# Kernel tuning notes

Measured on AMD Instinct MI355X. Metric: run time of the kernel, lower is better.

Reference implementation:

```python
import jax, jax.numpy as jnp
import numpy as np

B, S, D, E, H = 4, 2048, 1024, 8, 4096  # batch, seq, d_model, n_experts, ffn hidden (4*d_model)


def setup_inputs() -> dict:
    key = jax.random.key(0)
    ks = jax.random.split(key, 4)
    s = 0.02  # init scale
    return {
        "x": jax.random.normal(ks[0], (B, S, D), dtype=jnp.float32),
        "router_w": jax.random.normal(ks[1], (E, D), dtype=jnp.float32) * s,
        "router_b": jnp.zeros((E,), dtype=jnp.float32),
        "w1": jax.random.normal(ks[2], (E, D, H), dtype=jnp.float32) * s,
        "b1": jnp.zeros((E, H), dtype=jnp.float32),
        "w2": jax.random.normal(ks[3], (E, H, D), dtype=jnp.float32) * s,
        "b2": jnp.zeros((E, D), dtype=jnp.float32),
        "top_k": 2,
    }


def reference(x, router_w, router_b, w1, b1, w2, b2, top_k):
    # Router logits [B, S, E]
    logits = jnp.einsum('bsd,ed->bse', x, router_w) + router_b
    # Top-k selection; scatter top-k logits into a -inf tensor, then softmax
    # => gate weight is exactly 0 for non-selected experts.
    top_v, top_i = jax.lax.top_k(logits, top_k)           # [B, S, k]
    sel = jax.nn.one_hot(top_i, logits.shape[-1], dtype=bool).any(axis=-2)  # [B, S, E]
    gate = jax.nn.softmax(jnp.where(sel, logits, -jnp.inf), axis=-1)        # [B, S, E]

    # Dense sum over experts (mathematically identical to the masked
    # gather/scatter loop since non-selected gates are exactly 0).
    out = jnp.zeros_like(x)
    for e in range(w1.shape[0]):  # small fixed expert loop keeps peak memory low
        h = jax.nn.relu(x @ w1[e] + b1[e])        # [B, S, H]
        out = out + (h @ w2[e] + b2[e]) * gate[..., e:e + 1]
    return out
```

## Files before the change

kernel.cpp:

```cpp
#include <hip/hip_runtime.h>
#include <hip/hip_bf16.h>

#define NTOK   8192
#define DMODEL 1024
#define NEXP   8
#define HFFN   4096
#define NSLOT  16384
#define MAXWL  72

typedef __bf16 bf16x8 __attribute__((ext_vector_type(8)));
typedef float  f32x4  __attribute__((ext_vector_type(4)));
typedef unsigned short u16;
typedef u16 u16x8 __attribute__((ext_vector_type(8)));

typedef const __attribute__((address_space(1))) void* gas_ptr;
typedef __attribute__((address_space(3))) void* las_ptr;

__device__ inline u16 f2b(float f) {
  __hip_bfloat16 h = __float2bfloat16(f);
  return *reinterpret_cast<u16*>(&h);
}
__device__ inline float b2f(u16 u) {
  unsigned int v = ((unsigned int)u) << 16;
  return *reinterpret_cast<float*>(&v);
}

__global__ void router_k(const float* __restrict__ x, const float* __restrict__ rw,
                         const float* __restrict__ rb, int* __restrict__ tok_e,
                         float* __restrict__ tok_g) {
  int wave = threadIdx.x >> 6, lane = threadIdx.x & 63;
  int t = blockIdx.x * 4 + wave;
  const float* xr = x + (size_t)t * DMODEL;
  float acc[NEXP];
#pragma unroll
  for (int e = 0; e < NEXP; e++) acc[e] = 0.f;
#pragma unroll
  for (int i = 0; i < 4; i++) {
    int d = i * 256 + lane * 4;
    float4 xv = *(const float4*)(xr + d);
#pragma unroll
    for (int e = 0; e < NEXP; e++) {
      float4 wv = *(const float4*)(rw + (size_t)e * DMODEL + d);
      acc[e] += xv.x * wv.x + xv.y * wv.y + xv.z * wv.z + xv.w * wv.w;
    }
  }
#pragma unroll
  for (int e = 0; e < NEXP; e++) {
#pragma unroll
    for (int off = 32; off > 0; off >>= 1) acc[e] += __shfl_xor(acc[e], off);
  }
  if (lane == 0) {
    float lg[NEXP];
#pragma unroll
    for (int e = 0; e < NEXP; e++) lg[e] = acc[e] + rb[e];
    int e0 = 0;
#pragma unroll
    for (int e = 1; e < NEXP; e++) if (lg[e] > lg[e0]) e0 = e;
    int e1 = (e0 == 0) ? 1 : 0;
#pragma unroll
    for (int e = 0; e < NEXP; e++) if (e != e0 && lg[e] > lg[e1]) e1 = e;
    float ex = expf(lg[e1] - lg[e0]);
    float g0 = 1.f / (1.f + ex);
    float g1 = ex / (1.f + ex);
    tok_e[2 * t]     = e0;  tok_e[2 * t + 1] = e1;
    tok_g[2 * t]     = g0;  tok_g[2 * t + 1] = g1;
  }
}

__global__ void count_k(const int* __restrict__ tok_e, int* __restrict__ counts) {
  __shared__ int h[NEXP];
  int tid = threadIdx.x;
  if (tid < NEXP) h[tid] = 0;
  __syncthreads();
  int t = blockIdx.x * 256 + tid;
  atomicAdd(&h[tok_e[2 * t]], 1);
  atomicAdd(&h[tok_e[2 * t + 1]], 1);
  __syncthreads();
  if (tid < NEXP) atomicAdd(&counts[tid], h[tid]);
}

__global__ void offsets_k(const int* __restrict__ counts, int* __restrict__ offsets,
                          int* __restrict__ wl) {
  if (threadIdx.x == 0) {
    int s = 0;
    for (int e = 0; e < NEXP; e++) { offsets[e] = s; s += counts[e]; }
    offsets[NEXP] = s;
    int n = 0;
    for (int e = 0; e < NEXP; e++)
      for (int t = 0; t * 256 < counts[e]; ++t) wl[n++] = (e << 16) | t;
    for (int i = n; i < MAXWL; ++i) wl[i] = -1;
  }
}

__global__ void assign_k(const int* __restrict__ tok_e, int* __restrict__ cursors,
                         const int* __restrict__ offsets, int* __restrict__ row_tok,
                         int* __restrict__ slot_of) {
  __shared__ int h[NEXP], base[NEXP];
  int tid = threadIdx.x;
  if (tid < NEXP) h[tid] = 0;
  __syncthreads();
  int t = blockIdx.x * 256 + tid;
  int e0 = tok_e[2 * t], e1 = tok_e[2 * t + 1];
  int r0 = atomicAdd(&h[e0], 1);
  int r1 = atomicAdd(&h[e1], 1);
  __syncthreads();
  if (tid < NEXP) base[tid] = atomicAdd(&cursors[tid], h[tid]);
  __syncthreads();
  int s0 = offsets[e0] + base[e0] + r0;
  int s1 = offsets[e1] + base[e1] + r1;
  row_tok[s0] = t;  slot_of[2 * t] = s0;
  row_tok[s1] = t;  slot_of[2 * t + 1] = s1;
}

__global__ void gather_k(const float* __restrict__ x, const int* __restrict__ row_tok,
                         u16* __restrict__ xbg) {
  int idx = blockIdx.x * 256 + threadIdx.x;
  int s = idx >> 8;
  int c = (idx & 255) * 4;
  int t = row_tok[s];
  float4 v = *(const float4*)(x + (size_t)t * DMODEL + c);
  ushort4 o;
  o.x = f2b(v.x); o.y = f2b(v.y); o.z = f2b(v.z); o.w = f2b(v.w);
  *(ushort4*)(xbg + (size_t)s * DMODEL + c) = o;
}

__global__ void wtrans_k(const float* __restrict__ src, u16* __restrict__ dst,
                         int R, int C) {
  __shared__ u16 tile[64][72];
  int e = blockIdx.z;
  int r0 = blockIdx.x * 64, c0 = blockIdx.y * 64;
  int tid = threadIdx.x;
  int tr = tid >> 2, tc = (tid & 3) * 16;
  const float* sp = src + (size_t)e * R * C + (size_t)(r0 + tr) * C + c0 + tc;
#pragma unroll
  for (int i = 0; i < 16; i += 4) {
    float4 v = *(const float4*)(sp + i);
    tile[tr][tc + i]     = f2b(v.x);
    tile[tr][tc + i + 1] = f2b(v.y);
    tile[tr][tc + i + 2] = f2b(v.z);
    tile[tr][tc + i + 3] = f2b(v.w);
  }
  __syncthreads();
  u16* dbase = dst + (size_t)e * R * C;
#pragma unroll
  for (int it = 0; it < 2; ++it) {
    int oc  = it * 32 + (tid >> 3);
    int seg = (tid & 7) * 8;
    u16x8 o;
#pragma unroll
    for (int j = 0; j < 8; ++j) o[j] = tile[seg + j][oc];
    *(u16x8*)(dbase + (size_t)(c0 + oc) * R + r0 + seg) = o;
  }
}

template <int K, int NTOT, int NY, bool RELU>
__global__ __launch_bounds__(1024, 4) void moe_gemm_k(
    const u16* __restrict__ A, const u16* __restrict__ Bt,
    const float* __restrict__ bias, u16* __restrict__ Out,
    const int* __restrict__ counts, const int* __restrict__ offsets,
    const int* __restrict__ wl) {
  __shared__ __align__(16) u16 Als[3 * 8192];
  __shared__ __align__(16) u16 Bls[3 * 8192];

  int nwg = gridDim.x;
  int lid = blockIdx.x;
  int orig = (lid & 7) * (nwg >> 3) + (lid >> 3);
  int pair = orig / (MAXWL * 2);
  int rem  = orig - pair * (MAXWL * 2);
  int xt = rem >> 1;
  int y  = (pair << 1) | (rem & 1);
  int w = wl[xt];
  if (w < 0) return;
  int e   = w >> 16;
  int tr0 = (w & 0xffff) << 8;
  int cnt = counts[e];
  int seg = offsets[e];
  int n0  = y << 8;

  int tid = threadIdx.x;
  int wid = tid >> 6, lane = tid & 63;
  int wm = wid >> 2, wn = wid & 3;
  int l15 = lane & 15, lhi = lane >> 4;

  int co = (((tid & 3) ^ ((tid >> 3) & 3)) << 3);
  const u16* gA = A + (size_t)(seg + tr0 + (tid >> 2)) * K + co;
  const u16* gB = Bt + (size_t)e * NTOT * K + (size_t)(n0 + (tid >> 2)) * K + co;
  char* Ab = (char*)Als;
  char* Bb = (char*)Bls;
  int sdst = wid << 10;

  auto stage = [&](int bs, int kb) {
    __builtin_amdgcn_global_load_lds((gas_ptr)(gA + kb), (las_ptr)(Ab + bs * 16384 + sdst), 16, 0, 0);
    __builtin_amdgcn_global_load_lds((gas_ptr)(gB + kb), (las_ptr)(Bb + bs * 16384 + sdst), 16, 0, 0);
  };

  int xsw = ((lhi ^ ((l15 >> 1) & 3)) << 4);
  int aoff = (wm * 64 + l15) * 64 + xsw;
  int boff = (wn * 64 + l15) * 64 + xsw;

  constexpr int NT = K / 32;

  stage(0, 0);
  stage(1, 32);
  asm volatile("s_waitcnt vmcnt(2)" ::: "memory");
  __builtin_amdgcn_s_barrier();
  __builtin_amdgcn_sched_barrier(0);

  f32x4 acc[4][4] = {};
  int bufC = 0;
  for (int T = 0; T < NT; ++T) {
    int bufS = bufC + 2; if (bufS >= 3) bufS -= 3;
    bool ds = (T + 2 < NT);
    const char* ab = Ab + bufC * 16384;
    const char* bb = Bb + bufC * 16384;
    bf16x8 af[4], bv[4];
#pragma unroll
    for (int m = 0; m < 4; ++m) af[m] = *(const bf16x8*)(ab + aoff + m * 1024);
#pragma unroll
    for (int n = 0; n < 4; ++n) bv[n] = *(const bf16x8*)(bb + boff + n * 1024);
    if (ds) stage(bufS, (T + 2) * 32);
    __builtin_amdgcn_s_setprio(1);
#pragma unroll
    for (int m = 0; m < 4; ++m)
#pragma unroll
      for (int n = 0; n < 4; ++n)
        acc[m][n] = __builtin_amdgcn_mfma_f32_16x16x32_bf16(af[m], bv[n], acc[m][n], 0, 0, 0);
    __builtin_amdgcn_s_setprio(0);

    if (T + 1 < NT) {
      if (ds) asm volatile("s_waitcnt vmcnt(2)" ::: "memory");
      else    asm volatile("s_waitcnt vmcnt(0)" ::: "memory");
      __builtin_amdgcn_s_barrier();
      __builtin_amdgcn_sched_barrier(0);
    }
    bufC += 1; if (bufC >= 3) bufC -= 3;
  }

  const float* bias_e = bias + (size_t)e * NTOT;
  int cb = n0 + wn * 64 + l15;
  float bs4[4];
#pragma unroll
  for (int n = 0; n < 4; ++n) bs4[n] = bias_e[cb + n * 16];
  int rb0 = tr0 + wm * 64 + lhi * 4;
#pragma unroll
  for (int m = 0; m < 4; ++m) {
#pragma unroll
    for (int r2 = 0; r2 < 4; ++r2) {
      int gi = rb0 + m * 16 + r2;
      if (gi >= cnt) continue;
      size_t orow = (size_t)(seg + gi) * NTOT + cb;
#pragma unroll
      for (int n = 0; n < 4; ++n) {
        float v = acc[m][n][r2] + bs4[n];
        if (RELU) v = fmaxf(v, 0.f);
        Out[orow + n * 16] = f2b(v);
      }
    }
  }
}

__global__ void combine_k(const u16* __restrict__ Y, const int* __restrict__ slot_of,
                          const float* __restrict__ tok_g, float* __restrict__ out) {
  int t = blockIdx.x;
  int d = threadIdx.x * 4;
  int s0 = slot_of[2 * t], s1 = slot_of[2 * t + 1];
  float g0 = tok_g[2 * t], g1 = tok_g[2 * t + 1];
  ushort4 a = *(const ushort4*)(Y + (size_t)s0 * DMODEL + d);
  ushort4 b = *(const ushort4*)(Y + (size_t)s1 * DMODEL + d);
  float4 o;
  o.x = g0 * b2f(a.x) + g1 * b2f(b.x);
  o.y = g0 * b2f(a.y) + g1 * b2f(b.y);
  o.z = g0 * b2f(a.z) + g1 * b2f(b.z);
  o.w = g0 * b2f(a.w) + g1 * b2f(b.w);
  *(float4*)(out + (size_t)t * DMODEL + d) = o;
}

extern "C" void kernel_launch(void* const* d_in, const int* in_sizes, int n_in,
                              void* d_out, int out_size, void* d_ws, size_t ws_size,
                              hipStream_t stream) {
  const float* x  = (const float*)d_in[0];
  const float* rw = (const float*)d_in[1];
  const float* rb = (const float*)d_in[2];
  const float* w1 = (const float*)d_in[3];
  const float* b1 = (const float*)d_in[4];
  const float* w2 = (const float*)d_in[5];
  const float* b2 = (const float*)d_in[6];

  char* ws = (char*)d_ws;
  size_t o = 0;
  u16* w1t = (u16*)(ws + o); o += (size_t)NEXP * HFFN * DMODEL * 2;
  u16* w2t = (u16*)(ws + o); o += (size_t)NEXP * HFFN * DMODEL * 2;
  u16* xbg = (u16*)(ws + o); o += (size_t)(NSLOT + 256) * DMODEL * 2;
  u16* hc  = (u16*)(ws + o); o += (size_t)(NSLOT + 256) * HFFN * 2;
  u16* yb16 = (u16*)w1t;
  int*   tok_e   = (int*)(ws + o);   o += NTOK * 2 * sizeof(int);
  float* tok_g   = (float*)(ws + o); o += NTOK * 2 * sizeof(float);
  int*   slot_of = (int*)(ws + o);   o += NTOK * 2 * sizeof(int);
  int*   row_tok = (int*)(ws + o);   o += NSLOT * sizeof(int);
  int*   meta    = (int*)(ws + o);   o += 32 * sizeof(int);
  int*   wl      = (int*)(ws + o);   o += MAXWL * sizeof(int);
  int* counts  = meta;
  int* cursors = meta + 8;
  int* offsets = meta + 16;

  hipMemsetAsync(meta, 0, 64, stream);
  router_k<<<NTOK / 4, 256, 0, stream>>>(x, rw, rb, tok_e, tok_g);
  count_k<<<NTOK / 256, 256, 0, stream>>>(tok_e, counts);
  offsets_k<<<1, 64, 0, stream>>>(counts, offsets, wl);
  assign_k<<<NTOK / 256, 256, 0, stream>>>(tok_e, cursors, offsets, row_tok, slot_of);
  gather_k<<<NSLOT, 256, 0, stream>>>(x, row_tok, xbg);
  wtrans_k<<<dim3(DMODEL / 64, HFFN / 64, NEXP), 256, 0, stream>>>(w1, w1t, DMODEL, HFFN);
  wtrans_k<<<dim3(HFFN / 64, DMODEL / 64, NEXP), 256, 0, stream>>>(w2, w2t, HFFN, DMODEL);

  moe_gemm_k<DMODEL, HFFN, HFFN / 256, true>
      <<<MAXWL * (HFFN / 256), 1024, 0, stream>>>(
          xbg, w1t, b1, hc, counts, offsets, wl);
  moe_gemm_k<HFFN, DMODEL, DMODEL / 256, false>
      <<<MAXWL * (DMODEL / 256), 1024, 0, stream>>>(
          hc, w2t, b2, yb16, counts, offsets, wl);

  combine_k<<<NTOK, 256, 0, stream>>>(yb16, slot_of, tok_g, (float*)d_out);
}
```

Before: 545.0 us.

## Split-K second MoE GEMM, halve workgroup size, fold bias into combine

The grouped GEMM now runs 512-thread workgroups, and each wave computes a taller 128x64 slice with 8x4 accumulators, so every B fragment is reused across twice as many rows. The second GEMM splits K in two, doubling its grid to fill the GPU better. The two bf16 partial outputs are written to separate buffers and summed in the combine kernel, which also adds the b2 bias there. The cost is extra partial-output traffic, higher register pressure, and bf16 rounding of the partials before they are summed.

```diff
diff --git a/kernel.cpp b/kernel.cpp
--- a/kernel.cpp
+++ b/kernel.cpp
@@ -153,8 +153,8 @@
   }
 }
 
-template <int K, int NTOT, int NY, bool RELU>
-__global__ __launch_bounds__(1024, 4) void moe_gemm_k(
+template <int KTOT, int KCHUNK, int NTOT, int NY, int NKQ, bool RELU, bool BIAS>
+__global__ __launch_bounds__(512, 2) void moe_gemm_k(
     const u16* __restrict__ A, const u16* __restrict__ Bt,
     const float* __restrict__ bias, u16* __restrict__ Out,
     const int* __restrict__ counts, const int* __restrict__ offsets,
@@ -165,10 +165,12 @@
   int nwg = gridDim.x;
   int lid = blockIdx.x;
   int orig = (lid & 7) * (nwg >> 3) + (lid >> 3);
-  int pair = orig / (MAXWL * 2);
-  int rem  = orig - pair * (MAXWL * 2);
-  int xt = rem >> 1;
-  int y  = (pair << 1) | (rem & 1);
+  int kq   = orig / (MAXWL * NY);
+  int r1   = orig - kq * (MAXWL * NY);
+  int pair = r1 / (MAXWL * 2);
+  int r2   = r1 - pair * (MAXWL * 2);
+  int xt = r2 >> 1;
+  int y  = (pair << 1) | (r2 & 1);
   int w = wl[xt];
   if (w < 0) return;
   int e   = w >> 16;
@@ -182,31 +184,41 @@
   int wm = wid >> 2, wn = wid & 3;
   int l15 = lane & 15, lhi = lane >> 4;
 
-  int co = (((tid & 3) ^ ((tid >> 3) & 3)) << 3);
-  const u16* gA = A + (size_t)(seg + tr0 + (tid >> 2)) * K + co;
-  const u16* gB = Bt + (size_t)e * NTOT * K + (size_t)(n0 + (tid >> 2)) * K + co;
+  int co = (((tid & 3) ^ ((tid >> 3) & 3)) << 3) + kq * KCHUNK;
+  const u16* gA[2]; const u16* gB[2];
+  const u16* Bte = Bt + (size_t)e * NTOT * KTOT;
+#pragma unroll
+  for (int j = 0; j < 2; ++j) {
+    gA[j] = A + (size_t)(seg + tr0 + j * 128 + (tid >> 2)) * KTOT + co;
+    gB[j] = Bte + (size_t)(n0 + j * 128 + (tid >> 2)) * KTOT + co;
+  }
   char* Ab = (char*)Als;
   char* Bb = (char*)Bls;
   int sdst = wid << 10;
 
   auto stage = [&](int bs, int kb) {
-    __builtin_amdgcn_global_load_lds((gas_ptr)(gA + kb), (las_ptr)(Ab + bs * 16384 + sdst), 16, 0, 0);
-    __builtin_amdgcn_global_load_lds((gas_ptr)(gB + kb), (las_ptr)(Bb + bs * 16384 + sdst), 16, 0, 0);
+#pragma unroll
+    for (int j = 0; j < 2; ++j) {
+      __builtin_amdgcn_global_load_lds((gas_ptr)(gA[j] + kb),
+          (las_ptr)(Ab + bs * 16384 + j * 8192 + sdst), 16, 0, 0);
+      __builtin_amdgcn_global_load_lds((gas_ptr)(gB[j] + kb),
+          (las_ptr)(Bb + bs * 16384 + j * 8192 + sdst), 16, 0, 0);
+    }
   };
 
   int xsw = ((lhi ^ ((l15 >> 1) & 3)) << 4);
-  int aoff = (wm * 64 + l15) * 64 + xsw;
+  int aoff = (wm * 128 + l15) * 64 + xsw;
   int boff = (wn * 64 + l15) * 64 + xsw;
 
-  constexpr int NT = K / 32;
+  constexpr int NT = KCHUNK / 32;
 
   stage(0, 0);
   stage(1, 32);
-  asm volatile("s_waitcnt vmcnt(2)" ::: "memory");
+  asm volatile("s_waitcnt vmcnt(4)" ::: "memory");
   __builtin_amdgcn_s_barrier();
   __builtin_amdgcn_sched_barrier(0);
 
-  f32x4 acc[4][4] = {};
+  f32x4 acc[8][4] = {};
   int bufC = 0;
   for (int T = 0; T < NT; ++T) {
     int bufS = bufC + 2; if (bufS >= 3) bufS -= 3;
@@ -214,10 +226,11 @@
     const char* ab = Ab + bufC * 16384;
     const char* bb = Bb + bufC * 16384;
     bf16x8 af[4], bv[4];
+
+#pragma unroll
+    for (int n = 0; n < 4; ++n) bv[n] = *(const bf16x8*)(bb + boff + n * 1024);
 #pragma unroll
     for (int m = 0; m < 4; ++m) af[m] = *(const bf16x8*)(ab + aoff + m * 1024);
-#pragma unroll
-    for (int n = 0; n < 4; ++n) bv[n] = *(const bf16x8*)(bb + boff + n * 1024);
     if (ds) stage(bufS, (T + 2) * 32);
     __builtin_amdgcn_s_setprio(1);
 #pragma unroll
@@ -227,8 +240,18 @@
         acc[m][n] = __builtin_amdgcn_mfma_f32_16x16x32_bf16(af[m], bv[n], acc[m][n], 0, 0, 0);
     __builtin_amdgcn_s_setprio(0);
 
+#pragma unroll
+    for (int m = 0; m < 4; ++m) af[m] = *(const bf16x8*)(ab + aoff + (4 + m) * 1024);
+    __builtin_amdgcn_s_setprio(1);
+#pragma unroll
+    for (int m = 0; m < 4; ++m)
+#pragma unroll
+      for (int n = 0; n < 4; ++n)
+        acc[4 + m][n] = __builtin_amdgcn_mfma_f32_16x16x32_bf16(af[m], bv[n], acc[4 + m][n], 0, 0, 0);
+    __builtin_amdgcn_s_setprio(0);
+
     if (T + 1 < NT) {
-      if (ds) asm volatile("s_waitcnt vmcnt(2)" ::: "memory");
+      if (ds) asm volatile("s_waitcnt vmcnt(4)" ::: "memory");
       else    asm volatile("s_waitcnt vmcnt(0)" ::: "memory");
       __builtin_amdgcn_s_barrier();
       __builtin_amdgcn_sched_barrier(0);
@@ -236,42 +259,53 @@
     bufC += 1; if (bufC >= 3) bufC -= 3;
   }
 
-  const float* bias_e = bias + (size_t)e * NTOT;
+  u16* outp = Out + (size_t)kq * ((size_t)NSLOT * NTOT);
+
   int cb = n0 + wn * 64 + l15;
-  float bs4[4];
-#pragma unroll
-  for (int n = 0; n < 4; ++n) bs4[n] = bias_e[cb + n * 16];
-  int rb0 = tr0 + wm * 64 + lhi * 4;
-#pragma unroll
-  for (int m = 0; m < 4; ++m) {
-#pragma unroll
-    for (int r2 = 0; r2 < 4; ++r2) {
-      int gi = rb0 + m * 16 + r2;
+  float bs4[4] = {0.f, 0.f, 0.f, 0.f};
+  if (BIAS) {
+    const float* bias_e = bias + (size_t)e * NTOT;
+#pragma unroll
+    for (int n = 0; n < 4; ++n) bs4[n] = bias_e[cb + n * 16];
+  }
+  int rb0 = tr0 + wm * 128 + lhi * 4;
+#pragma unroll
+  for (int m = 0; m < 8; ++m) {
+#pragma unroll
+    for (int r = 0; r < 4; ++r) {
+      int gi = rb0 + m * 16 + r;
       if (gi >= cnt) continue;
       size_t orow = (size_t)(seg + gi) * NTOT + cb;
 #pragma unroll
       for (int n = 0; n < 4; ++n) {
-        float v = acc[m][n][r2] + bs4[n];
+        float v = acc[m][n][r] + bs4[n];
         if (RELU) v = fmaxf(v, 0.f);
-        Out[orow + n * 16] = f2b(v);
+        outp[orow + n * 16] = f2b(v);
       }
     }
   }
 }
 
 __global__ void combine_k(const u16* __restrict__ Y, const int* __restrict__ slot_of,
-                          const float* __restrict__ tok_g, float* __restrict__ out) {
+                          const int* __restrict__ tok_e, const float* __restrict__ tok_g,
+                          const float* __restrict__ b2, float* __restrict__ out) {
   int t = blockIdx.x;
   int d = threadIdx.x * 4;
   int s0 = slot_of[2 * t], s1 = slot_of[2 * t + 1];
+  int e0 = tok_e[2 * t],  e1 = tok_e[2 * t + 1];
   float g0 = tok_g[2 * t], g1 = tok_g[2 * t + 1];
-  ushort4 a = *(const ushort4*)(Y + (size_t)s0 * DMODEL + d);
-  ushort4 b = *(const ushort4*)(Y + (size_t)s1 * DMODEL + d);
+  const u16* Y1 = Y + (size_t)NSLOT * DMODEL;
+  ushort4 a0 = *(const ushort4*)(Y  + (size_t)s0 * DMODEL + d);
+  ushort4 a1 = *(const ushort4*)(Y1 + (size_t)s0 * DMODEL + d);
+  ushort4 c0 = *(const ushort4*)(Y  + (size_t)s1 * DMODEL + d);
+  ushort4 c1 = *(const ushort4*)(Y1 + (size_t)s1 * DMODEL + d);
+  float4 b20 = *(const float4*)(b2 + (size_t)e0 * DMODEL + d);
+  float4 b21 = *(const float4*)(b2 + (size_t)e1 * DMODEL + d);
   float4 o;
-  o.x = g0 * b2f(a.x) + g1 * b2f(b.x);
-  o.y = g0 * b2f(a.y) + g1 * b2f(b.y);
-  o.z = g0 * b2f(a.z) + g1 * b2f(b.z);
-  o.w = g0 * b2f(a.w) + g1 * b2f(b.w);
+  o.x = g0 * (b2f(a0.x) + b2f(a1.x) + b20.x) + g1 * (b2f(c0.x) + b2f(c1.x) + b21.x);
+  o.y = g0 * (b2f(a0.y) + b2f(a1.y) + b20.y) + g1 * (b2f(c0.y) + b2f(c1.y) + b21.y);
+  o.z = g0 * (b2f(a0.z) + b2f(a1.z) + b20.z) + g1 * (b2f(c0.z) + b2f(c1.z) + b21.z);
+  o.w = g0 * (b2f(a0.w) + b2f(a1.w) + b20.w) + g1 * (b2f(c0.w) + b2f(c1.w) + b21.w);
   *(float4*)(out + (size_t)t * DMODEL + d) = o;
 }
 
@@ -292,7 +326,7 @@
   u16* w2t = (u16*)(ws + o); o += (size_t)NEXP * HFFN * DMODEL * 2;
   u16* xbg = (u16*)(ws + o); o += (size_t)(NSLOT + 256) * DMODEL * 2;
   u16* hc  = (u16*)(ws + o); o += (size_t)(NSLOT + 256) * HFFN * 2;
-  u16* yb16 = (u16*)w1t;
+  u16* yp  = (u16*)w1t;
   int*   tok_e   = (int*)(ws + o);   o += NTOK * 2 * sizeof(int);
   float* tok_g   = (float*)(ws + o); o += NTOK * 2 * sizeof(float);
   int*   slot_of = (int*)(ws + o);   o += NTOK * 2 * sizeof(int);
@@ -312,12 +346,12 @@
   wtrans_k<<<dim3(DMODEL / 64, HFFN / 64, NEXP), 256, 0, stream>>>(w1, w1t, DMODEL, HFFN);
   wtrans_k<<<dim3(HFFN / 64, DMODEL / 64, NEXP), 256, 0, stream>>>(w2, w2t, HFFN, DMODEL);
 
-  moe_gemm_k<DMODEL, HFFN, HFFN / 256, true>
-      <<<MAXWL * (HFFN / 256), 1024, 0, stream>>>(
+  moe_gemm_k<DMODEL, DMODEL, HFFN, HFFN / 256, 1, true, true>
+      <<<MAXWL * (HFFN / 256), 512, 0, stream>>>(
           xbg, w1t, b1, hc, counts, offsets, wl);
-  moe_gemm_k<HFFN, DMODEL, DMODEL / 256, false>
-      <<<MAXWL * (DMODEL / 256), 1024, 0, stream>>>(
-          hc, w2t, b2, yb16, counts, offsets, wl);
-
-  combine_k<<<NTOK, 256, 0, stream>>>(yb16, slot_of, tok_g, (float*)d_out);
-}
+  moe_gemm_k<HFFN, HFFN / 2, DMODEL, DMODEL / 256, 2, false, false>
+      <<<MAXWL * (DMODEL / 256) * 2, 512, 0, stream>>>(
+          hc, w2t, nullptr, yp, counts, offsets, wl);
+
+  combine_k<<<NTOK, 256, 0, stream>>>(yp, slot_of, tok_e, tok_g, b2, (float*)d_out);
+}
```

Measured after the change: 588.8 us. +8.0%, slower.

## Split GEMM k-step into two phases interleaving A/B staging with MFMA halves

Applied to the files above, without the earlier changes.

Each k-iteration of the grouped expert GEMM now runs in two halves. The first half reads B fragments and the first two A fragments, issues the A global-to-LDS prefetch, barriers, then runs 8 MFMAs. The second half reads the remaining A fragments, issues the B prefetch, barriers, then runs the other 8 MFMAs. The aim is to spread LDS reads and global loads across the compute so they overlap better with MFMA work, in the style of ping-pong scheduling. The cost is two extra workgroup barriers per iteration, and the vmcnt accounting still assumes two loads in flight.

```diff
diff --git a/kernel.cpp b/kernel.cpp
--- a/kernel.cpp
+++ b/kernel.cpp
@@ -189,8 +189,10 @@
   char* Bb = (char*)Bls;
   int sdst = wid << 10;
 
-  auto stage = [&](int bs, int kb) {
+  auto stageA = [&](int bs, int kb) {
     __builtin_amdgcn_global_load_lds((gas_ptr)(gA + kb), (las_ptr)(Ab + bs * 16384 + sdst), 16, 0, 0);
+  };
+  auto stageB = [&](int bs, int kb) {
     __builtin_amdgcn_global_load_lds((gas_ptr)(gB + kb), (las_ptr)(Bb + bs * 16384 + sdst), 16, 0, 0);
   };
 
@@ -200,8 +202,8 @@
 
   constexpr int NT = K / 32;
 
-  stage(0, 0);
-  stage(1, 32);
+  stageA(0, 0);  stageB(0, 0);
+  stageA(1, 32); stageB(1, 32);
   asm volatile("s_waitcnt vmcnt(2)" ::: "memory");
   __builtin_amdgcn_s_barrier();
   __builtin_amdgcn_sched_barrier(0);
@@ -213,18 +215,37 @@
     bool ds = (T + 2 < NT);
     const char* ab = Ab + bufC * 16384;
     const char* bb = Bb + bufC * 16384;
-    bf16x8 af[4], bv[4];
-#pragma unroll
-    for (int m = 0; m < 4; ++m) af[m] = *(const bf16x8*)(ab + aoff + m * 1024);
+    int kb2 = (T + 2) * 32;
+    bf16x8 bv[4], af[2], ag[2];
+
 #pragma unroll
     for (int n = 0; n < 4; ++n) bv[n] = *(const bf16x8*)(bb + boff + n * 1024);
-    if (ds) stage(bufS, (T + 2) * 32);
+    af[0] = *(const bf16x8*)(ab + aoff);
+    af[1] = *(const bf16x8*)(ab + aoff + 1024);
+    if (ds) stageA(bufS, kb2);
+    __builtin_amdgcn_s_barrier();
+    asm volatile("s_waitcnt lgkmcnt(0)" ::: "memory");
+    __builtin_amdgcn_sched_barrier(0);
     __builtin_amdgcn_s_setprio(1);
 #pragma unroll
-    for (int m = 0; m < 4; ++m)
+    for (int m = 0; m < 2; ++m)
 #pragma unroll
       for (int n = 0; n < 4; ++n)
         acc[m][n] = __builtin_amdgcn_mfma_f32_16x16x32_bf16(af[m], bv[n], acc[m][n], 0, 0, 0);
+    __builtin_amdgcn_s_setprio(0);
+
+    ag[0] = *(const bf16x8*)(ab + aoff + 2 * 1024);
+    ag[1] = *(const bf16x8*)(ab + aoff + 3 * 1024);
+    if (ds) stageB(bufS, kb2);
+    __builtin_amdgcn_s_barrier();
+    asm volatile("s_waitcnt lgkmcnt(0)" ::: "memory");
+    __builtin_amdgcn_sched_barrier(0);
+    __builtin_amdgcn_s_setprio(1);
+#pragma unroll
+    for (int m = 0; m < 2; ++m)
+#pragma unroll
+      for (int n = 0; n < 4; ++n)
+        acc[2 + m][n] = __builtin_amdgcn_mfma_f32_16x16x32_bf16(ag[m], bv[n], acc[2 + m][n], 0, 0, 0);
     __builtin_amdgcn_s_setprio(0);
 
     if (T + 1 < NT) {
```

New measurement: 663.3 us. 21.7% more time.
